# Optimization experiments

Measured on AMD Instinct MI355X. Metric: run time of the kernel, lower is better.

The kernel has to match this reference:

```python
import jax, jax.numpy as jnp
import numpy as np

NUM_DOCS = 64
SENTS_PER_DOC = 512
HIDDEN = 256
HEADS = 4
NEG_SLOPE = 0.2  # DGL GATConv default leaky_relu slope


def setup_inputs() -> dict:
    key = jax.random.key(0)
    k1, k2, k3, k4 = jax.random.split(key, 4)
    N = NUM_DOCS * SENTS_PER_DOC
    scale = 1.0 / np.sqrt(HIDDEN)
    return {
        "sent_feature": jax.random.normal(k1, (N, HIDDEN), dtype=jnp.float32),
        "W": jax.random.normal(k2, (HIDDEN, HEADS * HIDDEN), dtype=jnp.float32) * scale,
        "attn_l": jax.random.normal(k3, (HEADS, HIDDEN), dtype=jnp.float32) * scale,
        "attn_r": jax.random.normal(k4, (HEADS, HIDDEN), dtype=jnp.float32) * scale,
        "bias": jnp.zeros((HEADS * HIDDEN,), dtype=jnp.float32),
        "num_docs": NUM_DOCS,
    }


def reference(sent_feature, W, attn_l, attn_r, bias, num_docs):
    # GATConv over a COMPLETE graph per document (self-loops included):
    # edge-softmax over all sources per destination == dense attention per doc block.
    N, F = sent_feature.shape
    B = num_docs
    S = N // B
    H, D = attn_l.shape  # num_heads, per-head out_feats
    # fc projection (no bias in DGL GATConv fc): [B, S, H, D]
    h = (sent_feature @ W).reshape(B, S, H, D)
    el = jnp.einsum("bshd,hd->bsh", h, attn_l)  # source term
    er = jnp.einsum("bshd,hd->bsh", h, attn_r)  # destination term
    # e[b, src, dst, h] = leaky_relu(el[src] + er[dst])
    e = jax.nn.leaky_relu(el[:, :, None, :] + er[:, None, :, :], NEG_SLOPE)
    # edge softmax: normalize over incoming edges (source axis) per destination
    alpha = jax.nn.softmax(e, axis=1)  # [B, S_src, S_dst, H]
    # scatter-reduce aggregation == dense contraction over sources
    out = jnp.einsum("bsth,bshd->bthd", alpha, h)  # [B, S_dst, H, D]
    out = out + bias.reshape(1, 1, H, D)
    # module returns sent_features.mean(dim=1) over heads
    return out.reshape(N, H, D).mean(axis=1)
```

## Files before the change

### kernel.cpp

```cpp
#include <hip/hip_runtime.h>
#include <hip/hip_bf16.h>

#define NDOCS 64
#define SS    512
#define FIN   256
#define NH    4
#define DD    256
#define NTOT  (NDOCS*SS)
#define HF    (NH*DD)
#define NEG   0.2f
#define LDA   264

typedef __attribute__((ext_vector_type(8))) short bf16x8;
typedef __attribute__((ext_vector_type(4))) float f32x4;

__device__ __forceinline__ unsigned short f2b(float x) {
    __hip_bfloat16 b = __float2bfloat16(x);
    return *reinterpret_cast<unsigned short*>(&b);
}
__device__ __forceinline__ unsigned pk2(float a, float b) {
    return (unsigned)f2b(a) | ((unsigned)f2b(b) << 16);
}
__device__ __forceinline__ float blo(unsigned u) {
    unsigned v = u << 16; return *reinterpret_cast<float*>(&v);
}
__device__ __forceinline__ float bhi(unsigned u) {
    unsigned v = u & 0xffff0000u; return *reinterpret_cast<float*>(&v);
}

#define BARLDS() do { asm volatile("s_waitcnt lgkmcnt(0)" ::: "memory"); \
                      __builtin_amdgcn_s_barrier(); } while (0)

__global__ __launch_bounds__(256) void k_wt(const float* __restrict__ W,
                                            unsigned short* __restrict__ WT) {
    int n  = blockIdx.x * 16 + (threadIdx.x & 15);
    int k0 = threadIdx.x >> 4;
#pragma unroll
    for (int i = 0; i < 16; i++) {
        int k = i * 16 + k0;
        WT[(size_t)n * FIN + k] = f2b(W[(size_t)k * HF + n]);
    }
}

__global__ __launch_bounds__(256) void k_fc(const float* __restrict__ X,
                                            const unsigned short* __restrict__ WT,
                                            const float* __restrict__ attn_l,
                                            const float* __restrict__ attn_r,
                                            unsigned short* __restrict__ hT,
                                            float* __restrict__ el,
                                            float* __restrict__ er) {
    __shared__ __align__(16) unsigned short Ald[64 * LDA];
    __shared__ float redl[4][64], redr[4][64];

    const int t    = threadIdx.x;
    const int mt64 = blockIdx.x >> 2;
    const int hh   = blockIdx.x & 3;
    const int row0 = mt64 * 64;
    const int w    = t >> 6;
    const int l    = t & 63;
    const int lr16 = l & 15;
    const int lg   = l >> 4;

    {
        const int c4   = (t & 63) * 4;
        const int rsub = t >> 6;
#pragma unroll
        for (int i = 0; i < 16; i++) {
            int r = i * 4 + rsub;
            float4 v = *reinterpret_cast<const float4*>(X + (size_t)(row0 + r) * FIN + c4);
            uint2 uu;
            uu.x = pk2(v.x, v.y);
            uu.y = pk2(v.z, v.w);
            *reinterpret_cast<uint2*>(&Ald[r * LDA + c4]) = uu;
        }
    }
    __syncthreads();

    f32x4 acc[4][4];
#pragma unroll
    for (int mt = 0; mt < 4; mt++)
#pragma unroll
        for (int nt = 0; nt < 4; nt++)
#pragma unroll
            for (int rg = 0; rg < 4; rg++) acc[mt][nt][rg] = 0.f;

    const unsigned short* wtb = WT + (size_t)(hh * DD + w * 64) * FIN;

#pragma unroll
    for (int kc = 0; kc < 8; kc++) {
        bf16x8 af[4], bv[4];
#pragma unroll
        for (int mt = 0; mt < 4; mt++)
            af[mt] = *reinterpret_cast<const bf16x8*>(
                &Ald[(mt * 16 + lr16) * LDA + kc * 32 + lg * 8]);
#pragma unroll
        for (int nt = 0; nt < 4; nt++)
            bv[nt] = *reinterpret_cast<const bf16x8*>(
                wtb + (size_t)(nt * 16 + lr16) * FIN + kc * 32 + lg * 8);
#pragma unroll
        for (int mt = 0; mt < 4; mt++)
#pragma unroll
            for (int nt = 0; nt < 4; nt++)
                acc[mt][nt] = __builtin_amdgcn_mfma_f32_16x16x32_bf16(
                    af[mt], bv[nt], acc[mt][nt], 0, 0, 0);
    }

    float al4[4], ar4[4];
#pragma unroll
    for (int nt = 0; nt < 4; nt++) {
        int d = w * 64 + nt * 16 + lr16;
        al4[nt] = attn_l[hh * DD + d];
        ar4[nt] = attn_r[hh * DD + d];
    }
#pragma unroll
    for (int mt = 0; mt < 4; mt++)
#pragma unroll
        for (int rg = 0; rg < 4; rg++) {
            float pl = 0.f, pr = 0.f;
#pragma unroll
            for (int nt = 0; nt < 4; nt++) {
                pl = fmaf(acc[mt][nt][rg], al4[nt], pl);
                pr = fmaf(acc[mt][nt][rg], ar4[nt], pr);
            }
#pragma unroll
            for (int off = 1; off < 16; off <<= 1) {
                pl += __shfl_xor(pl, off);
                pr += __shfl_xor(pr, off);
            }
            if (lr16 == 0) {
                int row = mt * 16 + lg * 4 + rg;
                redl[w][row] = pl;
                redr[w][row] = pr;
            }
        }
    __syncthreads();
    if (t < 64) {
        float sl = redl[0][t] + redl[1][t] + redl[2][t] + redl[3][t];
        float sr = redr[0][t] + redr[1][t] + redr[2][t] + redr[3][t];
        el[hh * NTOT + row0 + t] = sl;
        er[hh * NTOT + row0 + t] = sr;
    }

    {
        unsigned short* HL = Ald;
#pragma unroll
        for (int nt = 0; nt < 4; nt++) {
            int d = w * 64 + nt * 16 + lr16;
#pragma unroll
            for (int mt = 0; mt < 4; mt++) {
                int p = (mt * 4 + lg) ^ ((d & 7) << 1);
                ushort4 u;
                u.x = f2b(acc[mt][nt][0]);
                u.y = f2b(acc[mt][nt][1]);
                u.z = f2b(acc[mt][nt][2]);
                u.w = f2b(acc[mt][nt][3]);
                *reinterpret_cast<ushort4*>(HL + d * 64 + p * 4) = u;
            }
        }
        __syncthreads();
        const int bdoc  = row0 >> 9;
        const int sbase = row0 & 511;
        unsigned short* hTp = hT + ((size_t)(bdoc * NH + hh) * DD) * SS;
        const int dl = t >> 3, c = t & 7;
#pragma unroll
        for (int r = 0; r < 8; r++) {
            int d = r * 32 + dl;
            uint4 v = *reinterpret_cast<const uint4*>(HL + d * 64 + ((c ^ (d & 7)) << 3));
            *reinterpret_cast<uint4*>(hTp + (size_t)d * SS + sbase + c * 8) = v;
        }
    }
}

__global__ __launch_bounds__(256) void k_attn(const unsigned short* __restrict__ hT,
                                              const float* __restrict__ el,
                                              const float* __restrict__ er,
                                              const float* __restrict__ bias,
                                              float* __restrict__ out) {
    __shared__ __align__(16) unsigned short PT[2][64 * 64];
    __shared__ float els[SS];
    __shared__ float ers[64];
    __shared__ float esumL[4][64];
    __shared__ float rdenL[64];

    const int t    = threadIdx.x;
    const int b    = blockIdx.x & 63;
    const int tile = blockIdx.x >> 6;
    const int dst0 = tile * 64;
    const int w    = t >> 6;
    const int l    = t & 63;
    const int lr16 = l & 15;
    const int lg   = l >> 4;
    const int dstT = t & 63;
    const int sbT  = (t >> 6) * 16;

    f32x4 master[4][4];
#pragma unroll
    for (int mt = 0; mt < 4; mt++)
#pragma unroll
        for (int nt = 0; nt < 4; nt++)
#pragma unroll
            for (int r = 0; r < 4; r++) master[mt][nt][r] = 0.f;

    for (int hh = 0; hh < NH; hh++) {
        const unsigned short* hTw = hT + ((size_t)(b * NH + hh) * DD + w * 64) * SS;

        els[t]       = el[hh * NTOT + b * SS + t];
        els[t + 256] = el[hh * NTOT + b * SS + t + 256];
        if (t < 64) ers[t] = er[hh * NTOT + b * SS + dst0 + t];
        BARLDS();

        const float erv = ers[dstT];
        float myesum = 0.f;
        unsigned ecache[8][8];
#pragma unroll
        for (int c = 0; c < 8; c++)
#pragma unroll
            for (int jp = 0; jp < 8; jp++) {
                float x0 = els[c * 64 + sbT + 2 * jp]     + erv; x0 = x0 > 0.f ? x0 : NEG * x0;
                float x1 = els[c * 64 + sbT + 2 * jp + 1] + erv; x1 = x1 > 0.f ? x1 : NEG * x1;
                float e0 = __expf(x0), e1 = __expf(x1);
                myesum += e0 + e1;
                ecache[c][jp] = pk2(e0, e1);
            }
        esumL[w][dstT] = myesum;
        __syncthreads();
        if (t < 64)
            rdenL[t] = 1.f / (esumL[0][t] + esumL[1][t] + esumL[2][t] + esumL[3][t]);
        __syncthreads();
        const float rd = rdenL[dstT];

        bf16x8 bcur[4][2];
#pragma unroll
        for (int nt = 0; nt < 4; nt++)
#pragma unroll
            for (int ki = 0; ki < 2; ki++)
                bcur[nt][ki] = *reinterpret_cast<const bf16x8*>(
                    hTw + (size_t)(nt * 16 + lr16) * SS + (ki * 4 + lg) * 8);

#pragma unroll
        for (int c = 0; c < 8; c++) {
            const int cur = c & 1;
            {
                unsigned wb[8];
#pragma unroll
                for (int jp = 0; jp < 8; jp++)
                    wb[jp] = pk2(blo(ecache[c][jp]) * rd, bhi(ecache[c][jp]) * rd);
                int ds0   = (t >> 6) * 2;
                int slot0 = (ds0    ) ^ (dstT & 7);
                int slot1 = (ds0 + 1) ^ (dstT & 7);
                uint4 u0, u1;
                u0.x = wb[0]; u0.y = wb[1]; u0.z = wb[2]; u0.w = wb[3];
                u1.x = wb[4]; u1.y = wb[5]; u1.z = wb[6]; u1.w = wb[7];
                char* ptb = reinterpret_cast<char*>(&PT[cur][0]) + dstT * 128;
                *reinterpret_cast<uint4*>(ptb + slot0 * 16) = u0;
                *reinterpret_cast<uint4*>(ptb + slot1 * 16) = u1;
            }
            bf16x8 bnxt[4][2];
            if (c < 7) {
#pragma unroll
                for (int nt = 0; nt < 4; nt++)
#pragma unroll
                    for (int ki = 0; ki < 2; ki++)
                        bnxt[nt][ki] = *reinterpret_cast<const bf16x8*>(
                            hTw + (size_t)(nt * 16 + lr16) * SS + (c + 1) * 64 + (ki * 4 + lg) * 8);
            }
            BARLDS();
            const char* ptb = reinterpret_cast<const char*>(&PT[cur][0]);
#pragma unroll
            for (int ki = 0; ki < 2; ki++) {
                int ds = ki * 4 + lg;
                bf16x8 af[4];
#pragma unroll
                for (int mt = 0; mt < 4; mt++) {
                    int dst = mt * 16 + lr16;
                    af[mt] = *reinterpret_cast<const bf16x8*>(ptb + dst * 128 + ((ds ^ (dst & 7)) * 16));
                }
#pragma unroll
                for (int mt = 0; mt < 4; mt++)
#pragma unroll
                    for (int nt = 0; nt < 4; nt++)
                        master[mt][nt] = __builtin_amdgcn_mfma_f32_16x16x32_bf16(
                            af[mt], bcur[nt][ki], master[mt][nt], 0, 0, 0);
            }
            if (c < 7) {
#pragma unroll
                for (int nt = 0; nt < 4; nt++)
#pragma unroll
                    for (int ki = 0; ki < 2; ki++) bcur[nt][ki] = bnxt[nt][ki];
            }
        }
        __syncthreads();
    }

    float bs[4];
#pragma unroll
    for (int nt = 0; nt < 4; nt++) {
        int d = w * 64 + nt * 16 + lr16;
        float s = 0.f;
        for (int h2 = 0; h2 < NH; h2++) s += bias[h2 * DD + d];
        bs[nt] = s;
    }
#pragma unroll
    for (int mt = 0; mt < 4; mt++) {
        int rowb = b * SS + dst0 + mt * 16 + lg * 4;
#pragma unroll
        for (int nt = 0; nt < 4; nt++) {
            int d = w * 64 + nt * 16 + lr16;
#pragma unroll
            for (int rg = 0; rg < 4; rg++)
                out[(size_t)(rowb + rg) * DD + d] = 0.25f * (master[mt][nt][rg] + bs[nt]);
        }
    }
}

extern "C" void kernel_launch(void* const* d_in, const int* in_sizes, int n_in,
                              void* d_out, int out_size, void* d_ws, size_t ws_size,
                              hipStream_t stream) {
    const float* X      = (const float*)d_in[0];
    const float* W      = (const float*)d_in[1];
    const float* attn_l = (const float*)d_in[2];
    const float* attn_r = (const float*)d_in[3];
    const float* bias   = (const float*)d_in[4];

    unsigned short* hT = (unsigned short*)d_ws;
    float* elp = (float*)((char*)d_ws + (size_t)NTOT * HF * 2);
    float* erp = elp + (size_t)NH * NTOT;
    unsigned short* WTp = (unsigned short*)(erp + (size_t)NH * NTOT);
    float* outp = (float*)d_out;

    k_wt<<<64, 256, 0, stream>>>(W, WTp);
    k_fc<<<2048, 256, 0, stream>>>(X, WTp, attn_l, attn_r, hT, elp, erp);
    k_attn<<<NDOCS * 8, 256, 0, stream>>>(hT, elp, erp, bias, outp);
}
```

Measured before the change: 231.1 us.

## Halve attention dst tile and recompute exponentials to cut register pressure

The attention kernel now handles 32 destination rows per block instead of 64, doubling the grid, and declares a minimum of 4 blocks per CU in its launch bounds. The per-thread cache of packed exponentials is removed. Exponentials are computed once for the softmax denominator and again when writing the normalized weights, which frees registers. The aim is higher occupancy and better latency hiding. The cost is twice the total hT reads across blocks and repeated exp work. A trailing per-head barrier is also dropped.

```diff
diff --git a/kernel.cpp b/kernel.cpp
--- a/kernel.cpp
+++ b/kernel.cpp
@@ -21,12 +21,6 @@
 __device__ __forceinline__ unsigned pk2(float a, float b) {
     return (unsigned)f2b(a) | ((unsigned)f2b(b) << 16);
 }
-__device__ __forceinline__ float blo(unsigned u) {
-    unsigned v = u << 16; return *reinterpret_cast<float*>(&v);
-}
-__device__ __forceinline__ float bhi(unsigned u) {
-    unsigned v = u & 0xffff0000u; return *reinterpret_cast<float*>(&v);
-}
 
 #define BARLDS() do { asm volatile("s_waitcnt lgkmcnt(0)" ::: "memory"); \
                       __builtin_amdgcn_s_barrier(); } while (0)
@@ -171,31 +165,31 @@
     }
 }
 
-__global__ __launch_bounds__(256) void k_attn(const unsigned short* __restrict__ hT,
-                                              const float* __restrict__ el,
-                                              const float* __restrict__ er,
-                                              const float* __restrict__ bias,
-                                              float* __restrict__ out) {
-    __shared__ __align__(16) unsigned short PT[2][64 * 64];
+__global__ __launch_bounds__(256, 4) void k_attn(const unsigned short* __restrict__ hT,
+                                                 const float* __restrict__ el,
+                                                 const float* __restrict__ er,
+                                                 const float* __restrict__ bias,
+                                                 float* __restrict__ out) {
+    __shared__ __align__(16) unsigned short PT[2][32 * 64];
     __shared__ float els[SS];
-    __shared__ float ers[64];
-    __shared__ float esumL[4][64];
-    __shared__ float rdenL[64];
+    __shared__ float ers[32];
+    __shared__ float esumL[8][32];
+    __shared__ float rdenL[32];
 
     const int t    = threadIdx.x;
     const int b    = blockIdx.x & 63;
     const int tile = blockIdx.x >> 6;
-    const int dst0 = tile * 64;
+    const int dst0 = tile * 32;
     const int w    = t >> 6;
     const int l    = t & 63;
     const int lr16 = l & 15;
     const int lg   = l >> 4;
-    const int dstT = t & 63;
-    const int sbT  = (t >> 6) * 16;
-
-    f32x4 master[4][4];
-#pragma unroll
-    for (int mt = 0; mt < 4; mt++)
+    const int dstT = t & 31;
+    const int grpT = t >> 5;
+
+    f32x4 master[2][4];
+#pragma unroll
+    for (int mt = 0; mt < 2; mt++)
 #pragma unroll
         for (int nt = 0; nt < 4; nt++)
 #pragma unroll
@@ -206,26 +200,28 @@
 
         els[t]       = el[hh * NTOT + b * SS + t];
         els[t + 256] = el[hh * NTOT + b * SS + t + 256];
-        if (t < 64) ers[t] = er[hh * NTOT + b * SS + dst0 + t];
+        if (t < 32) ers[t] = er[hh * NTOT + b * SS + dst0 + t];
         BARLDS();
 
         const float erv = ers[dstT];
-        float myesum = 0.f;
-        unsigned ecache[8][8];
-#pragma unroll
-        for (int c = 0; c < 8; c++)
-#pragma unroll
-            for (int jp = 0; jp < 8; jp++) {
-                float x0 = els[c * 64 + sbT + 2 * jp]     + erv; x0 = x0 > 0.f ? x0 : NEG * x0;
-                float x1 = els[c * 64 + sbT + 2 * jp + 1] + erv; x1 = x1 > 0.f ? x1 : NEG * x1;
-                float e0 = __expf(x0), e1 = __expf(x1);
-                myesum += e0 + e1;
-                ecache[c][jp] = pk2(e0, e1);
-            }
-        esumL[w][dstT] = myesum;
+        {
+            float s0 = 0.f, s1 = 0.f;
+#pragma unroll
+            for (int s = 0; s < 64; s += 2) {
+                float x0 = els[grpT * 64 + s]     + erv; x0 = x0 > 0.f ? x0 : NEG * x0;
+                float x1 = els[grpT * 64 + s + 1] + erv; x1 = x1 > 0.f ? x1 : NEG * x1;
+                s0 += __expf(x0);
+                s1 += __expf(x1);
+            }
+            esumL[grpT][dstT] = s0 + s1;
+        }
         __syncthreads();
-        if (t < 64)
-            rdenL[t] = 1.f / (esumL[0][t] + esumL[1][t] + esumL[2][t] + esumL[3][t]);
+        if (t < 32) {
+            float s = 0.f;
+#pragma unroll
+            for (int g = 0; g < 8; g++) s += esumL[g][t];
+            rdenL[t] = 1.f / s;
+        }
         __syncthreads();
         const float rd = rdenL[dstT];
 
@@ -241,19 +237,19 @@
         for (int c = 0; c < 8; c++) {
             const int cur = c & 1;
             {
-                unsigned wb[8];
-#pragma unroll
-                for (int jp = 0; jp < 8; jp++)
-                    wb[jp] = pk2(blo(ecache[c][jp]) * rd, bhi(ecache[c][jp]) * rd);
-                int ds0   = (t >> 6) * 2;
-                int slot0 = (ds0    ) ^ (dstT & 7);
-                int slot1 = (ds0 + 1) ^ (dstT & 7);
-                uint4 u0, u1;
-                u0.x = wb[0]; u0.y = wb[1]; u0.z = wb[2]; u0.w = wb[3];
-                u1.x = wb[4]; u1.y = wb[5]; u1.z = wb[6]; u1.w = wb[7];
-                char* ptb = reinterpret_cast<char*>(&PT[cur][0]) + dstT * 128;
-                *reinterpret_cast<uint4*>(ptb + slot0 * 16) = u0;
-                *reinterpret_cast<uint4*>(ptb + slot1 * 16) = u1;
+                int sb = c * 64 + grpT * 8;
+                unsigned wb[4];
+#pragma unroll
+                for (int jp = 0; jp < 4; jp++) {
+                    float x0 = els[sb + 2 * jp]     + erv; x0 = x0 > 0.f ? x0 : NEG * x0;
+                    float x1 = els[sb + 2 * jp + 1] + erv; x1 = x1 > 0.f ? x1 : NEG * x1;
+                    wb[jp] = pk2(__expf(x0) * rd, __expf(x1) * rd);
+                }
+                int slot = grpT ^ (dstT & 7);
+                uint4 u;
+                u.x = wb[0]; u.y = wb[1]; u.z = wb[2]; u.w = wb[3];
+                *reinterpret_cast<uint4*>(
+                    reinterpret_cast<char*>(&PT[cur][0]) + dstT * 128 + slot * 16) = u;
             }
             bf16x8 bnxt[4][2];
             if (c < 7) {
@@ -269,14 +265,14 @@
 #pragma unroll
             for (int ki = 0; ki < 2; ki++) {
                 int ds = ki * 4 + lg;
-                bf16x8 af[4];
-#pragma unroll
-                for (int mt = 0; mt < 4; mt++) {
+                bf16x8 af[2];
+#pragma unroll
+                for (int mt = 0; mt < 2; mt++) {
                     int dst = mt * 16 + lr16;
                     af[mt] = *reinterpret_cast<const bf16x8*>(ptb + dst * 128 + ((ds ^ (dst & 7)) * 16));
                 }
 #pragma unroll
-                for (int mt = 0; mt < 4; mt++)
+                for (int mt = 0; mt < 2; mt++)
 #pragma unroll
                     for (int nt = 0; nt < 4; nt++)
                         master[mt][nt] = __builtin_amdgcn_mfma_f32_16x16x32_bf16(
@@ -289,7 +285,6 @@
                     for (int ki = 0; ki < 2; ki++) bcur[nt][ki] = bnxt[nt][ki];
             }
         }
-        __syncthreads();
     }
 
     float bs[4];
@@ -301,7 +296,7 @@
         bs[nt] = s;
     }
 #pragma unroll
-    for (int mt = 0; mt < 4; mt++) {
+    for (int mt = 0; mt < 2; mt++) {
         int rowb = b * SS + dst0 + mt * 16 + lg * 4;
 #pragma unroll
         for (int nt = 0; nt < 4; nt++) {
@@ -330,5 +325,5 @@
 
     k_wt<<<64, 256, 0, stream>>>(W, WTp);
     k_fc<<<2048, 256, 0, stream>>>(X, WTp, attn_l, attn_r, hT, elp, erp);
-    k_attn<<<NDOCS * 8, 256, 0, stream>>>(hT, elp, erp, bias, outp);
-}
+    k_attn<<<NDOCS * 16, 256, 0, stream>>>(hT, elp, erp, bias, outp);
+}
```

Measured after the change: 262.0 us. 13.4% more time.

## Compute attention weights in registers as MFMA B operand, defer softmax normalization

Applied to the files above, without the earlier changes.

The attention kernel no longer stages normalized probabilities through LDS with double-buffered barriers. Each wave now computes the exp(leaky_relu) weights directly into registers as the MFMA B operand, with hT as the A operand. Row sums are reduced with cross-lane shuffles and applied as a per-head scale after accumulation. This removes the separate exp prepass, the LDS round trip and most barriers, and stores output as float4 with launch bounds for two blocks per CU. In exchange it recomputes exponentials redundantly across waves, adds a second accumulator set that raises register pressure, and drops the explicit global-load prefetch.

```diff
diff --git a/kernel.cpp b/kernel.cpp
--- a/kernel.cpp
+++ b/kernel.cpp
@@ -21,15 +21,6 @@
 __device__ __forceinline__ unsigned pk2(float a, float b) {
     return (unsigned)f2b(a) | ((unsigned)f2b(b) << 16);
 }
-__device__ __forceinline__ float blo(unsigned u) {
-    unsigned v = u << 16; return *reinterpret_cast<float*>(&v);
-}
-__device__ __forceinline__ float bhi(unsigned u) {
-    unsigned v = u & 0xffff0000u; return *reinterpret_cast<float*>(&v);
-}
-
-#define BARLDS() do { asm volatile("s_waitcnt lgkmcnt(0)" ::: "memory"); \
-                      __builtin_amdgcn_s_barrier(); } while (0)
 
 __global__ __launch_bounds__(256) void k_wt(const float* __restrict__ W,
                                             unsigned short* __restrict__ WT) {
@@ -171,16 +162,12 @@
     }
 }
 
-__global__ __launch_bounds__(256) void k_attn(const unsigned short* __restrict__ hT,
-                                              const float* __restrict__ el,
-                                              const float* __restrict__ er,
-                                              const float* __restrict__ bias,
-                                              float* __restrict__ out) {
-    __shared__ __align__(16) unsigned short PT[2][64 * 64];
-    __shared__ float els[SS];
-    __shared__ float ers[64];
-    __shared__ float esumL[4][64];
-    __shared__ float rdenL[64];
+__global__ __launch_bounds__(256, 2) void k_attn(const unsigned short* __restrict__ hT,
+                                                 const float* __restrict__ el,
+                                                 const float* __restrict__ er,
+                                                 const float* __restrict__ bias,
+                                                 float* __restrict__ out) {
+    __shared__ __align__(16) float els[SS];
 
     const int t    = threadIdx.x;
     const int b    = blockIdx.x & 63;
@@ -190,127 +177,119 @@
     const int l    = t & 63;
     const int lr16 = l & 15;
     const int lg   = l >> 4;
-    const int dstT = t & 63;
-    const int sbT  = (t >> 6) * 16;
 
     f32x4 master[4][4];
 #pragma unroll
-    for (int mt = 0; mt < 4; mt++)
-#pragma unroll
-        for (int nt = 0; nt < 4; nt++)
-#pragma unroll
-            for (int r = 0; r < 4; r++) master[mt][nt][r] = 0.f;
+    for (int at = 0; at < 4; at++)
+#pragma unroll
+        for (int bt = 0; bt < 4; bt++)
+#pragma unroll
+            for (int r = 0; r < 4; r++) master[at][bt][r] = 0.f;
 
     for (int hh = 0; hh < NH; hh++) {
-        const unsigned short* hTw = hT + ((size_t)(b * NH + hh) * DD + w * 64) * SS;
-
+        __syncthreads();
         els[t]       = el[hh * NTOT + b * SS + t];
         els[t + 256] = el[hh * NTOT + b * SS + t + 256];
-        if (t < 64) ers[t] = er[hh * NTOT + b * SS + dst0 + t];
-        BARLDS();
-
-        const float erv = ers[dstT];
-        float myesum = 0.f;
-        unsigned ecache[8][8];
-#pragma unroll
-        for (int c = 0; c < 8; c++)
-#pragma unroll
-            for (int jp = 0; jp < 8; jp++) {
-                float x0 = els[c * 64 + sbT + 2 * jp]     + erv; x0 = x0 > 0.f ? x0 : NEG * x0;
-                float x1 = els[c * 64 + sbT + 2 * jp + 1] + erv; x1 = x1 > 0.f ? x1 : NEG * x1;
-                float e0 = __expf(x0), e1 = __expf(x1);
-                myesum += e0 + e1;
-                ecache[c][jp] = pk2(e0, e1);
-            }
-        esumL[w][dstT] = myesum;
         __syncthreads();
-        if (t < 64)
-            rdenL[t] = 1.f / (esumL[0][t] + esumL[1][t] + esumL[2][t] + esumL[3][t]);
-        __syncthreads();
-        const float rd = rdenL[dstT];
-
-        bf16x8 bcur[4][2];
-#pragma unroll
-        for (int nt = 0; nt < 4; nt++)
-#pragma unroll
-            for (int ki = 0; ki < 2; ki++)
-                bcur[nt][ki] = *reinterpret_cast<const bf16x8*>(
-                    hTw + (size_t)(nt * 16 + lr16) * SS + (ki * 4 + lg) * 8);
-
-#pragma unroll
+
+        float erv[4];
+#pragma unroll
+        for (int bt = 0; bt < 4; bt++)
+            erv[bt] = er[hh * NTOT + b * SS + dst0 + bt * 16 + lr16];
+
+        const unsigned short* hTw = hT + ((size_t)(b * NH + hh) * DD + w * 64) * SS;
+        const unsigned short* rowp[4];
+#pragma unroll
+        for (int at = 0; at < 4; at++)
+            rowp[at] = hTw + (size_t)(at * 16 + lr16) * SS + lg * 8;
+
+        float esum[4] = {0.f, 0.f, 0.f, 0.f};
+        f32x4 acch[4][4];
+#pragma unroll
+        for (int at = 0; at < 4; at++)
+#pragma unroll
+            for (int bt = 0; bt < 4; bt++)
+#pragma unroll
+                for (int r = 0; r < 4; r++) acch[at][bt][r] = 0.f;
+
+#pragma unroll 4
         for (int c = 0; c < 8; c++) {
-            const int cur = c & 1;
-            {
-                unsigned wb[8];
-#pragma unroll
-                for (int jp = 0; jp < 8; jp++)
-                    wb[jp] = pk2(blo(ecache[c][jp]) * rd, bhi(ecache[c][jp]) * rd);
-                int ds0   = (t >> 6) * 2;
-                int slot0 = (ds0    ) ^ (dstT & 7);
-                int slot1 = (ds0 + 1) ^ (dstT & 7);
-                uint4 u0, u1;
-                u0.x = wb[0]; u0.y = wb[1]; u0.z = wb[2]; u0.w = wb[3];
-                u1.x = wb[4]; u1.y = wb[5]; u1.z = wb[6]; u1.w = wb[7];
-                char* ptb = reinterpret_cast<char*>(&PT[cur][0]) + dstT * 128;
-                *reinterpret_cast<uint4*>(ptb + slot0 * 16) = u0;
-                *reinterpret_cast<uint4*>(ptb + slot1 * 16) = u1;
-            }
-            bf16x8 bnxt[4][2];
-            if (c < 7) {
-#pragma unroll
-                for (int nt = 0; nt < 4; nt++)
-#pragma unroll
-                    for (int ki = 0; ki < 2; ki++)
-                        bnxt[nt][ki] = *reinterpret_cast<const bf16x8*>(
-                            hTw + (size_t)(nt * 16 + lr16) * SS + (c + 1) * 64 + (ki * 4 + lg) * 8);
-            }
-            BARLDS();
-            const char* ptb = reinterpret_cast<const char*>(&PT[cur][0]);
 #pragma unroll
             for (int ki = 0; ki < 2; ki++) {
-                int ds = ki * 4 + lg;
+                const int s0 = c * 64 + ki * 32 + lg * 8;
                 bf16x8 af[4];
 #pragma unroll
-                for (int mt = 0; mt < 4; mt++) {
-                    int dst = mt * 16 + lr16;
-                    af[mt] = *reinterpret_cast<const bf16x8*>(ptb + dst * 128 + ((ds ^ (dst & 7)) * 16));
+                for (int at = 0; at < 4; at++)
+                    af[at] = *reinterpret_cast<const bf16x8*>(rowp[at] + c * 64 + ki * 32);
+                float4 e0 = *reinterpret_cast<const float4*>(&els[s0]);
+                float4 e1 = *reinterpret_cast<const float4*>(&els[s0 + 4]);
+                float e8[8] = {e0.x, e0.y, e0.z, e0.w, e1.x, e1.y, e1.z, e1.w};
+                bf16x8 bf[4];
+#pragma unroll
+                for (int bt = 0; bt < 4; bt++) {
+                    const float ev = erv[bt];
+                    unsigned u[4];
+#pragma unroll
+                    for (int jp = 0; jp < 4; jp++) {
+                        float x0 = e8[2 * jp]     + ev; x0 = x0 > 0.f ? x0 : NEG * x0;
+                        float x1 = e8[2 * jp + 1] + ev; x1 = x1 > 0.f ? x1 : NEG * x1;
+                        float ex0 = __expf(x0), ex1 = __expf(x1);
+                        esum[bt] += ex0 + ex1;
+                        u[jp] = pk2(ex0, ex1);
+                    }
+                    uint4 uu; uu.x = u[0]; uu.y = u[1]; uu.z = u[2]; uu.w = u[3];
+                    bf[bt] = *reinterpret_cast<bf16x8*>(&uu);
                 }
 #pragma unroll
-                for (int mt = 0; mt < 4; mt++)
-#pragma unroll
-                    for (int nt = 0; nt < 4; nt++)
-                        master[mt][nt] = __builtin_amdgcn_mfma_f32_16x16x32_bf16(
-                            af[mt], bcur[nt][ki], master[mt][nt], 0, 0, 0);
-            }
-            if (c < 7) {
-#pragma unroll
-                for (int nt = 0; nt < 4; nt++)
-#pragma unroll
-                    for (int ki = 0; ki < 2; ki++) bcur[nt][ki] = bnxt[nt][ki];
-            }
-        }
-        __syncthreads();
-    }
-
-    float bs[4];
-#pragma unroll
-    for (int nt = 0; nt < 4; nt++) {
-        int d = w * 64 + nt * 16 + lr16;
-        float s = 0.f;
-        for (int h2 = 0; h2 < NH; h2++) s += bias[h2 * DD + d];
-        bs[nt] = s;
-    }
-#pragma unroll
-    for (int mt = 0; mt < 4; mt++) {
-        int rowb = b * SS + dst0 + mt * 16 + lg * 4;
-#pragma unroll
-        for (int nt = 0; nt < 4; nt++) {
-            int d = w * 64 + nt * 16 + lr16;
-#pragma unroll
-            for (int rg = 0; rg < 4; rg++)
-                out[(size_t)(rowb + rg) * DD + d] = 0.25f * (master[mt][nt][rg] + bs[nt]);
-        }
-    }
+                for (int at = 0; at < 4; at++)
+#pragma unroll
+                    for (int bt = 0; bt < 4; bt++)
+                        acch[at][bt] = __builtin_amdgcn_mfma_f32_16x16x32_bf16(
+                            af[at], bf[bt], acch[at][bt], 0, 0, 0);
+            }
+        }
+
+        float rdn[4];
+#pragma unroll
+        for (int bt = 0; bt < 4; bt++) {
+            float s = esum[bt];
+            s += __shfl_xor(s, 16);
+            s += __shfl_xor(s, 32);
+            rdn[bt] = 1.f / s;
+        }
+#pragma unroll
+        for (int at = 0; at < 4; at++)
+#pragma unroll
+            for (int bt = 0; bt < 4; bt++)
+#pragma unroll
+                for (int r = 0; r < 4; r++)
+                    master[at][bt][r] = fmaf(rdn[bt], acch[at][bt][r], master[at][bt][r]);
+    }
+
+    float4 bs[4];
+#pragma unroll
+    for (int at = 0; at < 4; at++) {
+        float4 s = {0.f, 0.f, 0.f, 0.f};
+        for (int h2 = 0; h2 < NH; h2++) {
+            float4 v = *reinterpret_cast<const float4*>(
+                &bias[h2 * DD + w * 64 + at * 16 + lg * 4]);
+            s.x += v.x; s.y += v.y; s.z += v.z; s.w += v.w;
+        }
+        bs[at] = s;
+    }
+#pragma unroll
+    for (int at = 0; at < 4; at++)
+#pragma unroll
+        for (int bt = 0; bt < 4; bt++) {
+            int dst = dst0 + bt * 16 + lr16;
+            float4 o;
+            o.x = 0.25f * (master[at][bt][0] + bs[at].x);
+            o.y = 0.25f * (master[at][bt][1] + bs[at].y);
+            o.z = 0.25f * (master[at][bt][2] + bs[at].z);
+            o.w = 0.25f * (master[at][bt][3] + bs[at].w);
+            *reinterpret_cast<float4*>(
+                &out[(size_t)(b * SS + dst) * DD + w * 64 + at * 16 + lg * 4]) = o;
+        }
 }
 
 extern "C" void kernel_launch(void* const* d_in, const int* in_sizes, int n_in,
```

New measurement: 230.7 us. Within noise of the previous version (-0.2%).
